# Kernel optimization log

Measured on AMD Instinct MI355X. Metric: run time of the kernel, lower is better.

Reference implementation:

```python
import jax, jax.numpy as jnp
import numpy as np

B, H, K, V = 32, 32, 256, 256
CLIP = 1e6


def setup_inputs() -> dict:
    key = jax.random.key(0)
    k1, k2, k3, k4, k5 = jax.random.split(key, 5)
    state = jax.random.normal(k1, (B, H, K, V), dtype=jnp.float32)
    keys = jax.random.normal(k2, (B, H, K), dtype=jnp.float32)
    values = jax.random.normal(k3, (B, H, V), dtype=jnp.float32)
    gates = jax.random.uniform(k4, (B, H, K), dtype=jnp.float32)  # forget gates alpha in (0,1)
    beta = jax.random.uniform(k5, (B, H, 1), dtype=jnp.float32)   # learning rate beta in (0,1)
    return {"state": state, "keys": keys, "values": values, "gates": gates, "beta": beta}


def reference(state, keys, values, gates, beta):
    # KDA delta-rule update: S_t = (I - beta k k^T) Diag(alpha) S_{t-1} + beta k v^T
    state_decayed = gates[..., None] * state                       # (B,H,K,V)
    kt_state = jnp.einsum('bhk,bhkv->bhv', keys, state_decayed)    # k^T (Diag(a) S)
    beta_e = beta[..., None]                                       # (B,H,1,1)
    correction = beta_e * jnp.einsum('bhk,bhv->bhkv', keys, kt_state)
    kv_update = beta_e * jnp.einsum('bhk,bhv->bhkv', keys, values)
    new_state = state_decayed - correction + kv_update
    # NaN -> revert to previous state; Inf -> clip (matches torch module's checks)
    has_nan = jnp.isnan(new_state).any()
    has_inf = jnp.isinf(new_state).any()
    new_state = jnp.where(has_nan, state,
                          jnp.where(has_inf, jnp.clip(new_state, -CLIP, CLIP), new_state))
    return new_state
```

## Files before the change

### kernel.cpp

```cpp
#include <hip/hip_runtime.h>


#define KD 256
#define VD 256
#define SW 16

typedef float f32x4 __attribute__((ext_vector_type(4)));

__global__ __launch_bounds__(256, 4)
void kda_update_kernel(const float* __restrict__ state,
                       const float* __restrict__ keys,
                       const float* __restrict__ values,
                       const float* __restrict__ gates,
                       const float* __restrict__ beta,
                       float* __restrict__ out)
{
    const int bh    = blockIdx.x >> 2;
    const int slice = blockIdx.x & 3;
    const size_t tile_off = (size_t)bh * (KD * VD);
    const f32x4* __restrict__ S4 = (const f32x4*)(state + tile_off);
    f32x4* __restrict__ O4 = (f32x4*)(out + tile_off);

    __shared__ float s_g[KD];
    __shared__ float s_w[KD];
    __shared__ float s_c[KD];
    __shared__ f32x4 s_part[16][SW];
    __shared__ f32x4 s_kt[SW];

    const int t  = threadIdx.x;
    const int c  = t & (SW - 1);
    const int r0 = t >> 4;
    const int c0 = slice * SW;

    {
        const float g = gates[bh * KD + t];
        const float k = keys[bh * KD + t];
        s_g[t] = g;
        s_w[t] = g * k;
        s_c[t] = beta[bh] * k;
    }

    f32x4 s[16];
#pragma unroll
    for (int j = 0; j < 16; ++j) {
        s[j] = __builtin_nontemporal_load(&S4[(size_t)(r0 + 16 * j) * (VD / 4) + c0 + c]);
    }

    __syncthreads();

    f32x4 p = (f32x4)(0.f);
#pragma unroll
    for (int j = 0; j < 16; ++j) {
        const float w = s_w[r0 + 16 * j];
        p.x = fmaf(w, s[j].x, p.x);
        p.y = fmaf(w, s[j].y, p.y);
        p.z = fmaf(w, s[j].z, p.z);
        p.w = fmaf(w, s[j].w, p.w);
    }
    s_part[r0][c] = p;
    __syncthreads();

    if (t < SW) {
        f32x4 acc = s_part[0][t];
#pragma unroll
        for (int i = 1; i < 16; ++i) {
            const f32x4 q = s_part[i][t];
            acc.x += q.x; acc.y += q.y; acc.z += q.z; acc.w += q.w;
        }
        s_kt[t] = acc;
    }
    __syncthreads();

    const f32x4 kt = s_kt[c];
    const f32x4 vv = ((const f32x4*)(values + (size_t)bh * VD))[c0 + c];
    f32x4 d;
    d.x = vv.x - kt.x; d.y = vv.y - kt.y; d.z = vv.z - kt.z; d.w = vv.w - kt.w;

#pragma unroll
    for (int j = 0; j < 16; ++j) {
        const int k = r0 + 16 * j;
        const float g  = s_g[k];
        const float cb = s_c[k];
        f32x4 o;
        o.x = fmaf(g, s[j].x, cb * d.x);
        o.y = fmaf(g, s[j].y, cb * d.y);
        o.z = fmaf(g, s[j].z, cb * d.z);
        o.w = fmaf(g, s[j].w, cb * d.w);
        __builtin_nontemporal_store(o, &O4[(size_t)k * (VD / 4) + c0 + c]);
    }
}

extern "C" void kernel_launch(void* const* d_in, const int* in_sizes, int n_in,
                              void* d_out, int out_size, void* d_ws, size_t ws_size,
                              hipStream_t stream) {
    const float* state  = (const float*)d_in[0];
    const float* keys   = (const float*)d_in[1];
    const float* values = (const float*)d_in[2];
    const float* gates  = (const float*)d_in[3];
    const float* beta   = (const float*)d_in[4];
    float* out = (float*)d_out;

    dim3 grid(32 * 32 * 4);
    dim3 block(256);
    hipLaunchKernelGGL(kda_update_kernel, grid, block, 0, stream,
                       state, keys, values, gates, beta, out);
}
```

Baseline: 105.7 us.

## Process a full head per block with wave-level shuffle reduction

Launches one block per (batch, head) instead of four column-slice blocks. Each wave loops over four column groups and reduces the k^T S partial sums with cross-lane xor shuffles instead of shared-memory partials and two block barriers. Gate and beta*key are packed into one float2 shared array. The aim is to remove the LDS reduction and barrier cost. In exchange, each wave now touches only 64 contiguous bytes per row, which weakens coalescing. The four-iteration loop also serialises load, reduce and store inside each wave, which may hurt latency hiding on this bandwidth-bound update.

```diff
diff --git a/kernel.cpp b/kernel.cpp
--- a/kernel.cpp
+++ b/kernel.cpp
@@ -3,9 +3,10 @@
 
 #define KD 256
 #define VD 256
-#define SW 16
+#define VD4 (VD / 4)
 
 typedef float f32x4 __attribute__((ext_vector_type(4)));
+typedef float f32x2 __attribute__((ext_vector_type(2)));
 
 __global__ __launch_bounds__(256, 4)
 void kda_update_kernel(const float* __restrict__ state,
@@ -15,78 +16,77 @@
                        const float* __restrict__ beta,
                        float* __restrict__ out)
 {
-    const int bh    = blockIdx.x >> 2;
-    const int slice = blockIdx.x & 3;
-    const size_t tile_off = (size_t)bh * (KD * VD);
-    const f32x4* __restrict__ S4 = (const f32x4*)(state + tile_off);
-    f32x4* __restrict__ O4 = (f32x4*)(out + tile_off);
+    const int bh = blockIdx.x;
+    const size_t toff = (size_t)bh * (KD * VD);
+    const f32x4* __restrict__ S4 = (const f32x4*)(state + toff);
+    f32x4* __restrict__ O4 = (f32x4*)(out + toff);
+    const f32x4* __restrict__ V4 = (const f32x4*)(values + (size_t)bh * VD);
 
-    __shared__ float s_g[KD];
     __shared__ float s_w[KD];
-    __shared__ float s_c[KD];
-    __shared__ f32x4 s_part[16][SW];
-    __shared__ f32x4 s_kt[SW];
+    __shared__ f32x2 s_gc[KD];
 
-    const int t  = threadIdx.x;
-    const int c  = t & (SW - 1);
-    const int r0 = t >> 4;
-    const int c0 = slice * SW;
+    const int t    = threadIdx.x;
+    const int wv   = t >> 6;
+    const int lane = t & 63;
+    const int c    = lane & 3;
+    const int r0   = lane >> 2;
 
     {
         const float g = gates[bh * KD + t];
         const float k = keys[bh * KD + t];
-        s_g[t] = g;
         s_w[t] = g * k;
-        s_c[t] = beta[bh] * k;
-    }
-
-    f32x4 s[16];
-#pragma unroll
-    for (int j = 0; j < 16; ++j) {
-        s[j] = __builtin_nontemporal_load(&S4[(size_t)(r0 + 16 * j) * (VD / 4) + c0 + c]);
-    }
-
-    __syncthreads();
-
-    f32x4 p = (f32x4)(0.f);
-#pragma unroll
-    for (int j = 0; j < 16; ++j) {
-        const float w = s_w[r0 + 16 * j];
-        p.x = fmaf(w, s[j].x, p.x);
-        p.y = fmaf(w, s[j].y, p.y);
-        p.z = fmaf(w, s[j].z, p.z);
-        p.w = fmaf(w, s[j].w, p.w);
-    }
-    s_part[r0][c] = p;
-    __syncthreads();
-
-    if (t < SW) {
-        f32x4 acc = s_part[0][t];
-#pragma unroll
-        for (int i = 1; i < 16; ++i) {
-            const f32x4 q = s_part[i][t];
-            acc.x += q.x; acc.y += q.y; acc.z += q.z; acc.w += q.w;
-        }
-        s_kt[t] = acc;
+        f32x2 gc;
+        gc.x = g;
+        gc.y = beta[bh] * k;
+        s_gc[t] = gc;
     }
     __syncthreads();
 
-    const f32x4 kt = s_kt[c];
-    const f32x4 vv = ((const f32x4*)(values + (size_t)bh * VD))[c0 + c];
-    f32x4 d;
-    d.x = vv.x - kt.x; d.y = vv.y - kt.y; d.z = vv.z - kt.z; d.w = vv.w - kt.w;
+    for (int it = 0; it < 4; ++it) {
+        const int c4 = it * 16 + wv * 4 + c;
+
+        const f32x4 vv = V4[c4];
+
+        f32x4 s[16];
+#pragma unroll
+        for (int j = 0; j < 16; ++j)
+            s[j] = __builtin_nontemporal_load(&S4[(size_t)(r0 + 16 * j) * VD4 + c4]);
+
+        f32x4 p = (f32x4)(0.f);
+#pragma unroll
+        for (int j = 0; j < 16; ++j) {
+            const float w = s_w[r0 + 16 * j];
+            p.x = fmaf(w, s[j].x, p.x);
+            p.y = fmaf(w, s[j].y, p.y);
+            p.z = fmaf(w, s[j].z, p.z);
+            p.w = fmaf(w, s[j].w, p.w);
+        }
 
 #pragma unroll
-    for (int j = 0; j < 16; ++j) {
-        const int k = r0 + 16 * j;
-        const float g  = s_g[k];
-        const float cb = s_c[k];
-        f32x4 o;
-        o.x = fmaf(g, s[j].x, cb * d.x);
-        o.y = fmaf(g, s[j].y, cb * d.y);
-        o.z = fmaf(g, s[j].z, cb * d.z);
-        o.w = fmaf(g, s[j].w, cb * d.w);
-        __builtin_nontemporal_store(o, &O4[(size_t)k * (VD / 4) + c0 + c]);
+        for (int m = 4; m <= 32; m <<= 1) {
+            p.x += __shfl_xor(p.x, m, 64);
+            p.y += __shfl_xor(p.y, m, 64);
+            p.z += __shfl_xor(p.z, m, 64);
+            p.w += __shfl_xor(p.w, m, 64);
+        }
+
+        f32x4 d;
+        d.x = vv.x - p.x;
+        d.y = vv.y - p.y;
+        d.z = vv.z - p.z;
+        d.w = vv.w - p.w;
+
+#pragma unroll
+        for (int j = 0; j < 16; ++j) {
+            const int k = r0 + 16 * j;
+            const f32x2 gc = s_gc[k];
+            f32x4 o;
+            o.x = fmaf(gc.x, s[j].x, gc.y * d.x);
+            o.y = fmaf(gc.x, s[j].y, gc.y * d.y);
+            o.z = fmaf(gc.x, s[j].z, gc.y * d.z);
+            o.w = fmaf(gc.x, s[j].w, gc.y * d.w);
+            __builtin_nontemporal_store(o, &O4[(size_t)k * VD4 + c4]);
+        }
     }
 }
 
@@ -100,7 +100,7 @@
     const float* beta   = (const float*)d_in[4];
     float* out = (float*)d_out;
 
-    dim3 grid(32 * 32 * 4);
+    dim3 grid(32 * 32);
     dim3 block(256);
     hipLaunchKernelGGL(kda_update_kernel, grid, block, 0, stream,
                        state, keys, values, gates, beta, out);
```

Measured after the change: 231.1 us. 119% more time.
